# Kernel optimization log

Hardware: AMD Instinct MI355X
Metric: run time of the kernel (lower is better)

## Reference

```python
import jax, jax.numpy as jnp
import numpy as np

TOP_K = 3
EPS = 1e-12  # F.normalize eps


def _lstm(x, W_ih, W_hh, b_ih, b_hh):
    # x: [B, S, I]; PyTorch gate order i, f, g, o; returns h sequence [B, S, H]
    B = x.shape[0]
    H = W_hh.shape[1]
    xs = jnp.swapaxes(x, 0, 1)  # [S, B, I]
    x_proj = xs @ W_ih.T + b_ih + b_hh  # [S, B, 4H]

    def step(carry, xp):
        h, c = carry
        gates = xp + h @ W_hh.T
        i, f, g, o = jnp.split(gates, 4, axis=-1)
        i = jax.nn.sigmoid(i); f = jax.nn.sigmoid(f)
        g = jnp.tanh(g); o = jax.nn.sigmoid(o)
        c = f * c + i * g
        h = o * jnp.tanh(c)
        return (h, c), h

    init = (jnp.zeros((B, H), x.dtype), jnp.zeros((B, H), x.dtype))
    _, hs = jax.lax.scan(step, init, x_proj)
    return jnp.swapaxes(hs, 0, 1)  # [B, S, H]


def setup_inputs() -> dict:
    key = jax.random.key(0)
    ks = jax.random.split(key, 16)
    B, S, I, H, M, N, O = 4, 256, 512, 1024, 256, 65536, 512
    sc = 0.02
    return {
        "x": jax.random.normal(ks[0], (B, S, I), jnp.float32),
        "keys": jax.random.normal(ks[1], (N, M), jnp.float32),
        "values": jax.random.normal(ks[2], (N, M), jnp.float32),
        "importance": jnp.ones((N,), jnp.float32),
        "W_ih": jax.random.normal(ks[3], (4 * H, I), jnp.float32) * sc,
        "W_hh": jax.random.normal(ks[4], (4 * H, H), jnp.float32) * sc,
        "b_ih": jnp.zeros((4 * H,), jnp.float32),
        "b_hh": jnp.zeros((4 * H,), jnp.float32),
        "Wq": jax.random.normal(ks[5], (M, H), jnp.float32) * sc,
        "bq": jnp.zeros((M,), jnp.float32),
        "Wa": jax.random.normal(ks[6], (1, M), jnp.float32) * sc,
        "ba": jnp.zeros((1,), jnp.float32),
        "Wc": jax.random.normal(ks[7], (M, M), jnp.float32) * sc,
        "bc": jnp.zeros((M,), jnp.float32),
        "Wo": jax.random.normal(ks[8], (O, H + M), jnp.float32) * sc,
        "bo": jnp.zeros((O,), jnp.float32),
    }


def reference(x, keys, values, importance, W_ih, W_hh, b_ih, b_hh,
              Wq, bq, Wa, ba, Wc, bc, Wo, bo):
    # Controller LSTM over the whole sequence
    h = _lstm(x, W_ih, W_hh, b_ih, b_hh)  # [B, S, H]

    # Query projection and cosine similarity against the memory keys
    q = h @ Wq.T + bq  # [B, S, M]
    qn = q / jnp.maximum(jnp.linalg.norm(q, axis=-1, keepdims=True), EPS)
    kn = keys / jnp.maximum(jnp.linalg.norm(keys, axis=-1, keepdims=True), EPS)
    sim = jnp.einsum("bsm,nm->bsn", qn, kn) * importance  # [B, S, N]

    # Top-k retrieval and value gather
    _, top_idx = jax.lax.top_k(sim, TOP_K)  # [B, S, k]
    retrieved = values[top_idx]  # [B, S, k, M]

    # Learned attention over retrieved memories
    att_logits = (retrieved @ Wa.T + ba)[..., 0]  # [B, S, k]
    att = jax.nn.softmax(att_logits, axis=-1)
    mem = jnp.einsum("bsk,bskm->bsm", att, retrieved)
    mem = mem @ Wc.T + bc  # combine_layer

    out = jnp.concatenate([h, mem], axis=-1) @ Wo.T + bo  # [B, S, O]
    return out
```

## Files before the change

kernel.cpp:

```cpp
#include <hip/hip_runtime.h>
#include <hip/hip_bf16.h>
#include <cstdint>
#include <cstddef>

#define BB 4
#define SS 256
#define ID 512
#define HD 1024
#define MD 256
#define NKEY 65536
#define OD 512
#define ROWS 1024
#define NWG_LSTM 256
#define NTH_LSTM 256
#define KPB 2048
#define KSPLITS (NKEY / KPB)

typedef __attribute__((ext_vector_type(8))) short bf16x8;
typedef __attribute__((ext_vector_type(4))) float f32x4;
typedef __attribute__((ext_vector_type(8))) unsigned short u16x8;

__global__ __launch_bounds__(256) void sgemm_nt(
    const float* __restrict__ A, int lda,
    const float* __restrict__ Bm, int ldb,
    float* __restrict__ C, int ldc, int K,
    const float* __restrict__ bias, const float* __restrict__ bias2,
    int accum)
{
    __shared__ float As[64][17];
    __shared__ float Bs[64][17];
    const int t = threadIdx.x;
    const int tx = t & 15, ty = t >> 4;
    const int bm = blockIdx.y << 6, bn = blockIdx.x << 6;
    const int lrow = t >> 2, lk4 = (t & 3) << 2;
    float acc[4][4] = {};

    for (int kb = 0; kb < K; kb += 16) {
        const float4 av = *(const float4*)&A[(size_t)(bm + lrow) * lda + kb + lk4];
        const float4 bv = *(const float4*)&Bm[(size_t)(bn + lrow) * ldb + kb + lk4];
        __syncthreads();
        As[lrow][lk4 + 0] = av.x; As[lrow][lk4 + 1] = av.y;
        As[lrow][lk4 + 2] = av.z; As[lrow][lk4 + 3] = av.w;
        Bs[lrow][lk4 + 0] = bv.x; Bs[lrow][lk4 + 1] = bv.y;
        Bs[lrow][lk4 + 2] = bv.z; Bs[lrow][lk4 + 3] = bv.w;
        __syncthreads();
#pragma unroll
        for (int k = 0; k < 16; ++k) {
            const float a0 = As[4 * ty + 0][k], a1 = As[4 * ty + 1][k];
            const float a2 = As[4 * ty + 2][k], a3 = As[4 * ty + 3][k];
            const float b0 = Bs[4 * tx + 0][k], b1 = Bs[4 * tx + 1][k];
            const float b2 = Bs[4 * tx + 2][k], b3 = Bs[4 * tx + 3][k];
            acc[0][0] += a0 * b0; acc[0][1] += a0 * b1; acc[0][2] += a0 * b2; acc[0][3] += a0 * b3;
            acc[1][0] += a1 * b0; acc[1][1] += a1 * b1; acc[1][2] += a1 * b2; acc[1][3] += a1 * b3;
            acc[2][0] += a2 * b0; acc[2][1] += a2 * b1; acc[2][2] += a2 * b2; acc[2][3] += a2 * b3;
            acc[3][0] += a3 * b0; acc[3][1] += a3 * b1; acc[3][2] += a3 * b2; acc[3][3] += a3 * b3;
        }
    }

#pragma unroll
    for (int i = 0; i < 4; ++i) {
        const int row = bm + 4 * ty + i;
        const int col = bn + 4 * tx;
        float4* cp = (float4*)&C[(size_t)row * ldc + col];
        float4 r;
        if (accum) {
            const float4 old = *cp;
            r.x = old.x + acc[i][0]; r.y = old.y + acc[i][1];
            r.z = old.z + acc[i][2]; r.w = old.w + acc[i][3];
        } else {
            float bx = bias[col + 0], by = bias[col + 1], bz = bias[col + 2], bw = bias[col + 3];
            if (bias2) { bx += bias2[col + 0]; by += bias2[col + 1]; bz += bias2[col + 2]; bw += bias2[col + 3]; }
            r.x = acc[i][0] + bx; r.y = acc[i][1] + by;
            r.z = acc[i][2] + bz; r.w = acc[i][3] + bw;
        }
        *cp = r;
    }
}

__global__ __launch_bounds__(256) void sgemm_nt_w(
    const float* __restrict__ A, const float* __restrict__ Bm,
    float* __restrict__ C, const float* __restrict__ bias, const float* __restrict__ bias2)
{
    __shared__ float As[16][64];
    __shared__ float Bs[16][128];
    const int t = threadIdx.x;
    const int tx = t & 15, ty = t >> 4;
    const int bm = blockIdx.y << 6, bn = blockIdx.x << 7;
    const int arow = t & 63, akq = t >> 6;
    const int brow = t & 127, bkq = t >> 7;
    float acc[4][8] = {};

    for (int kb = 0; kb < 512; kb += 16) {
        const float4 av  = *(const float4*)&A[(size_t)(bm + arow) * 512 + kb + (akq << 2)];
        const float4 bv0 = *(const float4*)&Bm[(size_t)(bn + brow) * 512 + kb + (bkq << 3)];
        const float4 bv1 = *(const float4*)&Bm[(size_t)(bn + brow) * 512 + kb + (bkq << 3) + 4];
        __syncthreads();
        As[(akq << 2) + 0][arow] = av.x; As[(akq << 2) + 1][arow] = av.y;
        As[(akq << 2) + 2][arow] = av.z; As[(akq << 2) + 3][arow] = av.w;
        Bs[(bkq << 3) + 0][brow] = bv0.x; Bs[(bkq << 3) + 1][brow] = bv0.y;
        Bs[(bkq << 3) + 2][brow] = bv0.z; Bs[(bkq << 3) + 3][brow] = bv0.w;
        Bs[(bkq << 3) + 4][brow] = bv1.x; Bs[(bkq << 3) + 5][brow] = bv1.y;
        Bs[(bkq << 3) + 6][brow] = bv1.z; Bs[(bkq << 3) + 7][brow] = bv1.w;
        __syncthreads();
#pragma unroll
        for (int k = 0; k < 16; ++k) {
            const float4 a  = *(const float4*)&As[k][ty << 2];
            const float4 b0 = *(const float4*)&Bs[k][tx << 3];
            const float4 b1 = *(const float4*)&Bs[k][(tx << 3) + 4];
            acc[0][0] += a.x * b0.x; acc[0][1] += a.x * b0.y; acc[0][2] += a.x * b0.z; acc[0][3] += a.x * b0.w;
            acc[0][4] += a.x * b1.x; acc[0][5] += a.x * b1.y; acc[0][6] += a.x * b1.z; acc[0][7] += a.x * b1.w;
            acc[1][0] += a.y * b0.x; acc[1][1] += a.y * b0.y; acc[1][2] += a.y * b0.z; acc[1][3] += a.y * b0.w;
            acc[1][4] += a.y * b1.x; acc[1][5] += a.y * b1.y; acc[1][6] += a.y * b1.z; acc[1][7] += a.y * b1.w;
            acc[2][0] += a.z * b0.x; acc[2][1] += a.z * b0.y; acc[2][2] += a.z * b0.z; acc[2][3] += a.z * b0.w;
            acc[2][4] += a.z * b1.x; acc[2][5] += a.z * b1.y; acc[2][6] += a.z * b1.z; acc[2][7] += a.z * b1.w;
            acc[3][0] += a.w * b0.x; acc[3][1] += a.w * b0.y; acc[3][2] += a.w * b0.z; acc[3][3] += a.w * b0.w;
            acc[3][4] += a.w * b1.x; acc[3][5] += a.w * b1.y; acc[3][6] += a.w * b1.z; acc[3][7] += a.w * b1.w;
        }
    }

#pragma unroll
    for (int i = 0; i < 4; ++i) {
        const int row = bm + (ty << 2) + i;
        const int col = bn + (tx << 3);
        float4 r0, r1;
        r0.x = acc[i][0] + bias[col + 0] + bias2[col + 0];
        r0.y = acc[i][1] + bias[col + 1] + bias2[col + 1];
        r0.z = acc[i][2] + bias[col + 2] + bias2[col + 2];
        r0.w = acc[i][3] + bias[col + 3] + bias2[col + 3];
        r1.x = acc[i][4] + bias[col + 4] + bias2[col + 4];
        r1.y = acc[i][5] + bias[col + 5] + bias2[col + 5];
        r1.z = acc[i][6] + bias[col + 6] + bias2[col + 6];
        r1.w = acc[i][7] + bias[col + 7] + bias2[col + 7];
        *(float4*)&C[(size_t)row * 4096 + col] = r0;
        *(float4*)&C[(size_t)row * 4096 + col + 4] = r1;
    }
}

__device__ inline unsigned pack_bf16(float a, float b) {
    return (__float_as_uint(a) >> 16) | (__float_as_uint(b) & 0xFFFF0000u);
}

__global__ void rownorm(const float* __restrict__ X, float* __restrict__ Xn, int nrows)
{
    const int row = blockIdx.x * 4 + (threadIdx.x >> 6);
    const int lane = threadIdx.x & 63;
    if (row >= nrows) return;
    float4 v = *(const float4*)&X[(size_t)row * 256 + (lane << 2)];
    float ss = v.x * v.x + v.y * v.y + v.z * v.z + v.w * v.w;
#pragma unroll
    for (int o = 1; o < 64; o <<= 1) ss += __shfl_xor(ss, o);
    const float sc = 1.f / fmaxf(sqrtf(ss), 1e-12f);
    v.x *= sc; v.y *= sc; v.z *= sc; v.w *= sc;
    *(float4*)&Xn[(size_t)row * 256 + (lane << 2)] = v;
}

__device__ inline float sigm_f(float x) { return 1.f / (1.f + __expf(-x)); }
__device__ inline float tanh_f(float x) { return 1.f - 2.f / (__expf(2.f * x) + 1.f); }

#define SUBSTEP(B, U, UN, C4, XPC) do {                                           \
    asm volatile("s_waitcnt vmcnt(3)" ::: "memory");                              \
    __builtin_amdgcn_sched_barrier(0);                                            \
    const unsigned* pb_ = rec + (slot << 12) + (B << 10) + (t << 2);              \
    while ((((U.x ^ st) | (U.y ^ st) | (U.z ^ st) | (U.w ^ st)) & 0xFFu) != 0u) { \
        __builtin_amdgcn_s_sleep(1);                                              \
        asm volatile("global_load_dwordx4 %0, %1, off sc0 sc1\n\ts_waitcnt vmcnt(0)" \
                     : "=&v"(U) : "v"(pb_) : "memory");                           \
    }                                                                             \
    {                                                                             \
        float4 hw_;                                                               \
        hw_.x = __uint_as_float(U.x & 0xFFFFFF00u);                               \
        hw_.y = __uint_as_float(U.y & 0xFFFFFF00u);                               \
        hw_.z = __uint_as_float(U.z & 0xFFFFFF00u);                               \
        hw_.w = __uint_as_float(U.w & 0xFFFFFF00u);                               \
        *(float4*)&h_lds[B][t << 2] = hw_;                                        \
    }                                                                             \
    asm volatile("s_waitcnt lgkmcnt(0)" ::: "memory");                            \
    __builtin_amdgcn_sched_barrier(0);                                            \
    __builtin_amdgcn_s_barrier();                                                 \
    {                                                                             \
        const unsigned* pn_ = rec + (((B == 3) ? (slot ^ 1) : slot) << 12)        \
                              + (((B + 1) & 3) << 10) + (t << 2);                 \
        asm volatile("global_load_dwordx4 %0, %1, off sc0 sc1"                    \
                     : "=&v"(UN) : "v"(pn_) : "memory");                          \
    }                                                                             \
    const float* hb_ = &h_lds[B][0];                                              \
    float ax_ = 0.f, ay_ = 0.f, az_ = 0.f, aw_ = 0.f;                             \
    _Pragma("unroll")                                                             \
    for (int j = 0; j < 16; ++j) {                                                \
        const float4 hv_ = *(const float4*)&hb_[(ksub << 2) + (j << 6)];          \
        ax_ += w4[j].x * hv_.x; ay_ += w4[j].y * hv_.y;                           \
        az_ += w4[j].z * hv_.z; aw_ += w4[j].w * hv_.w;                           \
    }                                                                             \
    float sm_ = (ax_ + ay_) + (az_ + aw_);                                        \
    sm_ += __shfl_xor(sm_, 1); sm_ += __shfl_xor(sm_, 2);                         \
    sm_ += __shfl_xor(sm_, 4); sm_ += __shfl_xor(sm_, 8);                         \
    sm_ += XPC;                                                                   \
    const float vi_ = __shfl(sm_, ksub);                                          \
    const float vf_ = __shfl(sm_, ksub + 16);                                     \
    const float vg_ = __shfl(sm_, ksub + 32);                                     \
    const float vo_ = __shfl(sm_, ksub + 48);                                     \
    const float iv_ = sigm_f(vi_), fv_ = sigm_f(vf_);                             \
    const float gv_ = tanh_f(vg_), ov_ = sigm_f(vo_);                             \
    C4 = fv_ * C4 + iv_ * gv_;                                                    \
    const float hvv_ = ov_ * tanh_f(C4);                                          \
    if (lane == 0) {                                                              \
        unsigned* dst_ = rec + ((slot ^ 1) << 12) + (B << 10) + unit;             \
        const unsigned uv_ = (__float_as_uint(hvv_) & 0xFFFFFF00u) |              \
                             ((unsigned)(s + 1) & 0xFFu);                         \
        float* ha_ = &h_all[(size_t)((B << 8) + s) * 1024 + unit];                \
        asm volatile("global_store_dword %0, %1, off sc0 sc1"                     \
                     :: "v"(dst_), "v"(uv_) : "memory");                          \
        asm volatile("global_store_dword %0, %1, off"                             \
                     :: "v"(ha_), "v"(hvv_) : "memory");                          \
    }                                                                             \
    {                                                                             \
        const float* px_ = &xp[(size_t)((B << 8) + sn) * 4096 + wrow];            \
        asm volatile("global_load_dword %0, %1, off"                              \
                     : "=&v"(XPC) : "v"(px_) : "memory");                         \
    }                                                                             \
} while (0)

__global__ __launch_bounds__(256) void lstm_kernel(
    const float* __restrict__ xp, const float* __restrict__ W_hh,
    unsigned* __restrict__ rec, float* __restrict__ h_all,
    const float* __restrict__ keys, const float* __restrict__ imp,
    float* __restrict__ rnk, unsigned short* __restrict__ kb)
{
    __shared__ float h_lds[4][1024];
    const int t = threadIdx.x;

    if (blockIdx.x >= NWG_LSTM) {
        const int base_row = (blockIdx.x - NWG_LSTM) << 8;
        const int lane = t & 63;
        for (int it = 0; it < 64; ++it) {
            const int row = base_row + (it << 2) + (t >> 6);
            float4 v = *(const float4*)&keys[(size_t)row * 256 + (lane << 2)];
            float ss = v.x * v.x + v.y * v.y + v.z * v.z + v.w * v.w;
#pragma unroll
            for (int o = 1; o < 64; o <<= 1) ss += __shfl_xor(ss, o);
            const float sc = imp[row] / fmaxf(sqrtf(ss), 1e-12f);
            if (lane == 0) rnk[row] = sc;
            if (kb) {
                uint2 p;
                p.x = pack_bf16(v.x * sc, v.y * sc);
                p.y = pack_bf16(v.z * sc, v.w * sc);
                *(uint2*)&kb[(size_t)row * 256 + (lane << 2)] = p;
            }
        }
        return;
    }

    const int wave = t >> 6, lane = t & 63;
    const int gt = lane >> 4, ksub = lane & 15;
    const int unit = (blockIdx.x << 2) + wave;
    const int wrow = (gt << 10) + unit;

    float4 w4[16];
#pragma unroll
    for (int j = 0; j < 16; ++j)
        w4[j] = *(const float4*)&W_hh[(size_t)wrow * 1024 + (ksub << 2) + (j << 6)];

    float c40 = 0.f, c41 = 0.f, c42 = 0.f, c43 = 0.f;
    float xpc0 = xp[(size_t)(0 * 256 + 0) * 4096 + wrow];
    float xpc1 = xp[(size_t)(1 * 256 + 0) * 4096 + wrow];
    float xpc2 = xp[(size_t)(2 * 256 + 0) * 4096 + wrow];
    float xpc3 = xp[(size_t)(3 * 256 + 0) * 4096 + wrow];

    uint4 u0 = make_uint4(~0u, ~0u, ~0u, ~0u);
    uint4 u1 = u0, u2 = u0, u3 = u0;

    {
        const unsigned* p00 = rec + (t << 2);
        asm volatile("global_load_dwordx4 %0, %1, off sc0 sc1\n\ts_waitcnt vmcnt(0)"
                     : "=&v"(u0) : "v"(p00) : "memory");
        __builtin_amdgcn_sched_barrier(0);
    }

    for (int s = 0; s < 256; ++s) {
        const int slot = s & 1;
        const unsigned st = (unsigned)s & 0xFFu;
        const int sn = (s < 255) ? s + 1 : 255;
        SUBSTEP(0, u0, u1, c40, xpc0);
        SUBSTEP(1, u1, u2, c41, xpc1);
        SUBSTEP(2, u2, u3, c42, xpc2);
        SUBSTEP(3, u3, u0, c43, xpc3);
    }
}

#define SWAP1(A, B, IA, IB) { float _t = A; A = B; B = _t; int _u = IA; IA = IB; IB = _u; }
#define INS8G(P, V, ID) do {                                          \
    const float _v = (V); const int _id = (ID);                       \
    if (_v > P##v7) {                                                 \
        P##v7 = _v; P##i7 = _id;                                      \
        if (P##v7 > P##v6) SWAP1(P##v6, P##v7, P##i6, P##i7);         \
        if (P##v6 > P##v5) SWAP1(P##v5, P##v6, P##i5, P##i6);         \
        if (P##v5 > P##v4) SWAP1(P##v4, P##v5, P##i4, P##i5);         \
        if (P##v4 > P##v3) SWAP1(P##v3, P##v4, P##i3, P##i4);         \
        if (P##v3 > P##v2) SWAP1(P##v2, P##v3, P##i2, P##i3);         \
        if (P##v2 > P##v1) SWAP1(P##v1, P##v2, P##i1, P##i2);         \
        if (P##v1 > P##v0) SWAP1(P##v0, P##v1, P##i0, P##i1);         \
    }                                                                 \
} while (0)
#define DECL8(P) float P##v0=-3e38f,P##v1=-3e38f,P##v2=-3e38f,P##v3=-3e38f, \
                       P##v4=-3e38f,P##v5=-3e38f,P##v6=-3e38f,P##v7=-3e38f; \
                 int P##i0=0x7fffffff,P##i1=0x7fffffff,P##i2=0x7fffffff,P##i3=0x7fffffff, \
                     P##i4=0x7fffffff,P##i5=0x7fffffff,P##i6=0x7fffffff,P##i7=0x7fffffff;

__global__ __launch_bounds__(512) void sim_mfma_b8(
    const float* __restrict__ qn, const unsigned short* __restrict__ kb,
    float* __restrict__ part_v8, int* __restrict__ part_i8)
{
    __shared__ unsigned short k_lds[64 * 264];
    const int t = threadIdx.x;
    const int wave = t >> 6, lane = t & 63;
    const int ks = blockIdx.x, qs = blockIdx.y;
    const int key_base = ks * KPB;
    const int q0 = qs << 7;
    const int qrow = q0 + (wave << 4) + (lane & 15);
    const int kg = lane >> 4;

    bf16x8 bq[8];
#pragma unroll
    for (int kc = 0; kc < 8; ++kc) {
        const float* qp = &qn[(size_t)qrow * 256 + (kc << 5) + (kg << 3)];
        const float4 f0 = *(const float4*)qp;
        const float4 f1 = *(const float4*)(qp + 4);
        union { unsigned int u[4]; bf16x8 h; } cv;
        cv.u[0] = pack_bf16(f0.x, f0.y);
        cv.u[1] = pack_bf16(f0.z, f0.w);
        cv.u[2] = pack_bf16(f1.x, f1.y);
        cv.u[3] = pack_bf16(f1.z, f1.w);
        bq[kc] = cv.h;
    }

    DECL8(t)

    const int srow = t >> 3, scol0 = (t & 7) << 5;

    for (int stg = 0; stg < KPB / 64; ++stg) {
        __syncthreads();
        {
            const unsigned short* kp = &kb[(size_t)(key_base + (stg << 6) + srow) * 256 + scol0];
#pragma unroll
            for (int i = 0; i < 4; ++i)
                *(u16x8*)&k_lds[srow * 264 + scol0 + (i << 3)] = *(const u16x8*)(kp + (i << 3));
        }
        __syncthreads();

#pragma unroll
        for (int kt = 0; kt < 4; ++kt) {
            f32x4 a0 = {0.f, 0.f, 0.f, 0.f};
            f32x4 a1 = {0.f, 0.f, 0.f, 0.f};
#pragma unroll
            for (int kc = 0; kc < 4; ++kc) {
                const bf16x8 af = *(const bf16x8*)&k_lds[((kt << 4) + (lane & 15)) * 264 +
                                                         (kc << 5) + (kg << 3)];
                a0 = __builtin_amdgcn_mfma_f32_16x16x32_bf16(af, bq[kc], a0, 0, 0, 0);
            }
#pragma unroll
            for (int kc = 4; kc < 8; ++kc) {
                const bf16x8 af = *(const bf16x8*)&k_lds[((kt << 4) + (lane & 15)) * 264 +
                                                         (kc << 5) + (kg << 3)];
                a1 = __builtin_amdgcn_mfma_f32_16x16x32_bf16(af, bq[kc], a1, 0, 0, 0);
            }
            const int kidx = key_base + (stg << 6) + (kt << 4) + (kg << 2);
            INS8G(t, a0[0] + a1[0], kidx + 0);
            INS8G(t, a0[1] + a1[1], kidx + 1);
            INS8G(t, a0[2] + a1[2], kidx + 2);
            INS8G(t, a0[3] + a1[3], kidx + 3);
        }
    }

    float* cand_v = (float*)k_lds;
    int*   cand_i = (int*)(k_lds + 8192);
    __syncthreads();
    cand_v[t * 8 + 0] = tv0; cand_i[t * 8 + 0] = ti0;
    cand_v[t * 8 + 1] = tv1; cand_i[t * 8 + 1] = ti1;
    cand_v[t * 8 + 2] = tv2; cand_i[t * 8 + 2] = ti2;
    cand_v[t * 8 + 3] = tv3; cand_i[t * 8 + 3] = ti3;
    cand_v[t * 8 + 4] = tv4; cand_i[t * 8 + 4] = ti4;
    cand_v[t * 8 + 5] = tv5; cand_i[t * 8 + 5] = ti5;
    cand_v[t * 8 + 6] = tv6; cand_i[t * 8 + 6] = ti6;
    cand_v[t * 8 + 7] = tv7; cand_i[t * 8 + 7] = ti7;
    __syncthreads();
    if (t < 128) {
        DECL8(m)
        const int w = t >> 4, c = t & 15;
        for (int g = 0; g < 4; ++g) {
            const int src = ((w << 6) + (g << 4) + c) * 8;
            for (int r = 0; r < 8; ++r)
                INS8G(m, cand_v[src + r], cand_i[src + r]);
        }
        const size_t base = (size_t)(q0 + t) * (KSPLITS * 8) + ks * 8;
        part_v8[base + 0] = mv0; part_i8[base + 0] = mi0;
        part_v8[base + 1] = mv1; part_i8[base + 1] = mi1;
        part_v8[base + 2] = mv2; part_i8[base + 2] = mi2;
        part_v8[base + 3] = mv3; part_i8[base + 3] = mi3;
        part_v8[base + 4] = mv4; part_i8[base + 4] = mi4;
        part_v8[base + 5] = mv5; part_i8[base + 5] = mi5;
        part_v8[base + 6] = mv6; part_i8[base + 6] = mi6;
        part_v8[base + 7] = mv7; part_i8[base + 7] = mi7;
    }
}

__global__ __launch_bounds__(256) void sim_mfma_f(
    const float* __restrict__ qn, const float* __restrict__ keys,
    const float* __restrict__ rnk, float* __restrict__ part_v8, int* __restrict__ part_i8)
{
    __shared__ unsigned short k_lds[64 * 264];
    __shared__ float cand_v[256 * 8];
    __shared__ int   cand_i[256 * 8];
    const int t = threadIdx.x;
    const int wave = t >> 6, lane = t & 63;
    const int ks = blockIdx.x, qs = blockIdx.y;
    const int key_base = ks * KPB;
    const int q0 = qs << 6;
    const int qrow = q0 + (wave << 4) + (lane & 15);
    const int kg = lane >> 4;

    bf16x8 bq[8];
#pragma unroll
    for (int kc = 0; kc < 8; ++kc) {
        const float* qp = &qn[(size_t)qrow * 256 + (kc << 5) + (kg << 3)];
        const float4 f0 = *(const float4*)qp;
        const float4 f1 = *(const float4*)(qp + 4);
        union { unsigned int u[4]; bf16x8 h; } cv;
        cv.u[0] = pack_bf16(f0.x, f0.y);
        cv.u[1] = pack_bf16(f0.z, f0.w);
        cv.u[2] = pack_bf16(f1.x, f1.y);
        cv.u[3] = pack_bf16(f1.z, f1.w);
        bq[kc] = cv.h;
    }

    DECL8(t)

    for (int stg = 0; stg < KPB / 64; ++stg) {
        __syncthreads();
#pragma unroll
        for (int i = 0; i < 8; ++i) {
            const int g = (i << 11) + (t << 3);
            const int row = g >> 8, col = g & 255;
            const int krow = key_base + (stg << 6) + row;
            const float sc = rnk[krow];
            const float* kp = &keys[(size_t)krow * 256 + col];
            float4 f0 = *(const float4*)kp;
            float4 f1 = *(const float4*)(kp + 4);
            f0.x *= sc; f0.y *= sc; f0.z *= sc; f0.w *= sc;
            f1.x *= sc; f1.y *= sc; f1.z *= sc; f1.w *= sc;
            union { unsigned int u[4]; u16x8 h; } cv;
            cv.u[0] = pack_bf16(f0.x, f0.y);
            cv.u[1] = pack_bf16(f0.z, f0.w);
            cv.u[2] = pack_bf16(f1.x, f1.y);
            cv.u[3] = pack_bf16(f1.z, f1.w);
            *(u16x8*)&k_lds[row * 264 + col] = cv.h;
        }
        __syncthreads();

#pragma unroll
        for (int kt = 0; kt < 4; ++kt) {
            f32x4 a0 = {0.f, 0.f, 0.f, 0.f};
            f32x4 a1 = {0.f, 0.f, 0.f, 0.f};
#pragma unroll
            for (int kc = 0; kc < 4; ++kc) {
                const bf16x8 af = *(const bf16x8*)&k_lds[((kt << 4) + (lane & 15)) * 264 +
                                                         (kc << 5) + (kg << 3)];
                a0 = __builtin_amdgcn_mfma_f32_16x16x32_bf16(af, bq[kc], a0, 0, 0, 0);
            }
#pragma unroll
            for (int kc = 4; kc < 8; ++kc) {
                const bf16x8 af = *(const bf16x8*)&k_lds[((kt << 4) + (lane & 15)) * 264 +
                                                         (kc << 5) + (kg << 3)];
                a1 = __builtin_amdgcn_mfma_f32_16x16x32_bf16(af, bq[kc], a1, 0, 0, 0);
            }
            const int kidx = key_base + (stg << 6) + (kt << 4) + (kg << 2);
            INS8G(t, a0[0] + a1[0], kidx + 0);
            INS8G(t, a0[1] + a1[1], kidx + 1);
            INS8G(t, a0[2] + a1[2], kidx + 2);
            INS8G(t, a0[3] + a1[3], kidx + 3);
        }
    }

    __syncthreads();
    cand_v[t * 8 + 0] = tv0; cand_i[t * 8 + 0] = ti0;
    cand_v[t * 8 + 1] = tv1; cand_i[t * 8 + 1] = ti1;
    cand_v[t * 8 + 2] = tv2; cand_i[t * 8 + 2] = ti2;
    cand_v[t * 8 + 3] = tv3; cand_i[t * 8 + 3] = ti3;
    cand_v[t * 8 + 4] = tv4; cand_i[t * 8 + 4] = ti4;
    cand_v[t * 8 + 5] = tv5; cand_i[t * 8 + 5] = ti5;
    cand_v[t * 8 + 6] = tv6; cand_i[t * 8 + 6] = ti6;
    cand_v[t * 8 + 7] = tv7; cand_i[t * 8 + 7] = ti7;
    __syncthreads();
    if (t < 64) {
        DECL8(m)
        const int w = t >> 4, c = t & 15;
        for (int g = 0; g < 4; ++g) {
            const int src = ((w << 6) + c + (g << 4)) * 8;
            for (int r = 0; r < 8; ++r)
                INS8G(m, cand_v[src + r], cand_i[src + r]);
        }
        const size_t base = (size_t)(q0 + t) * (KSPLITS * 8) + ks * 8;
        part_v8[base + 0] = mv0; part_i8[base + 0] = mi0;
        part_v8[base + 1] = mv1; part_i8[base + 1] = mi1;
        part_v8[base + 2] = mv2; part_i8[base + 2] = mi2;
        part_v8[base + 3] = mv3; part_i8[base + 3] = mi3;
        part_v8[base + 4] = mv4; part_i8[base + 4] = mi4;
        part_v8[base + 5] = mv5; part_i8[base + 5] = mi5;
        part_v8[base + 6] = mv6; part_i8[base + 6] = mi6;
        part_v8[base + 7] = mv7; part_i8[base + 7] = mi7;
    }
}

__global__ __launch_bounds__(256) void cand_merge(
    const float* __restrict__ part_v8, const int* __restrict__ part_i8,
    int* __restrict__ cand8_i)
{
    __shared__ float pv[256 * 8];
    __shared__ int   pi[256 * 8];
    const int t = threadIdx.x;
    const int qq = t >> 3, sl = t & 7;
    const int q = (blockIdx.x << 5) + qq;
    {
        DECL8(p)
        const size_t base = (size_t)q * (KSPLITS * 8) + sl * 32;
        for (int j = 0; j < 32; ++j)
            INS8G(p, part_v8[base + j], part_i8[base + j]);
        pv[t * 8 + 0] = pv0; pi[t * 8 + 0] = pi0;
        pv[t * 8 + 1] = pv1; pi[t * 8 + 1] = pi1;
        pv[t * 8 + 2] = pv2; pi[t * 8 + 2] = pi2;
        pv[t * 8 + 3] = pv3; pi[t * 8 + 3] = pi3;
        pv[t * 8 + 4] = pv4; pi[t * 8 + 4] = pi4;
        pv[t * 8 + 5] = pv5; pi[t * 8 + 5] = pi5;
        pv[t * 8 + 6] = pv6; pi[t * 8 + 6] = pi6;
        pv[t * 8 + 7] = pv7; pi[t * 8 + 7] = pi7;
    }
    __syncthreads();
    if (sl == 0) {
        DECL8(c)
        const int b0 = (qq << 3) * 8;
        for (int j = 0; j < 64; ++j)
            INS8G(c, pv[b0 + j], pi[b0 + j]);
        cand8_i[q * 8 + 0] = ci0; cand8_i[q * 8 + 1] = ci1;
        cand8_i[q * 8 + 2] = ci2; cand8_i[q * 8 + 3] = ci3;
        cand8_i[q * 8 + 4] = ci4; cand8_i[q * 8 + 5] = ci5;
        cand8_i[q * 8 + 6] = ci6; cand8_i[q * 8 + 7] = ci7;
    }
}

__global__ void rescore_gather(const float* __restrict__ qn, const float* __restrict__ keys,
                               const float* __restrict__ rnk, const int* __restrict__ cand8_i,
                               const float* __restrict__ values, const float* __restrict__ Wa,
                               const float* __restrict__ ba, float* __restrict__ mem_raw)
{
    const int q = blockIdx.x;
    const int lane = threadIdx.x;
    const float4 qv = *(const float4*)&qn[(size_t)q * 256 + (lane << 2)];
    float s0, s1, s2, s3, s4, s5, s6, s7;
    int j0, j1, j2, j3, j4, j5, j6, j7;
#define RES(R, S, J) { J = cand8_i[q * 8 + R]; \
    const float4 kv = *(const float4*)&keys[(size_t)J * 256 + (lane << 2)]; \
    float d = qv.x * kv.x + qv.y * kv.y + qv.z * kv.z + qv.w * kv.w; \
    d += __shfl_xor(d, 1); d += __shfl_xor(d, 2); d += __shfl_xor(d, 4); \
    d += __shfl_xor(d, 8); d += __shfl_xor(d, 16); d += __shfl_xor(d, 32); \
    S = d * rnk[J]; }
    RES(0, s0, j0) RES(1, s1, j1) RES(2, s2, j2) RES(3, s3, j3)
    RES(4, s4, j4) RES(5, s5, j5) RES(6, s6, j6) RES(7, s7, j7)
#undef RES
    int top[3];
#define BET(SV, JV) if (SV > bv || (SV == bv && JV < bi)) { bv = SV; bi = JV; }
#pragma unroll
    for (int k = 0; k < 3; ++k) {
        float bv = s0; int bi = j0;
        BET(s1, j1) BET(s2, j2) BET(s3, j3) BET(s4, j4)
        BET(s5, j5) BET(s6, j6) BET(s7, j7)
        top[k] = bi;
        if (j0 == bi) s0 = -3e38f;
        if (j1 == bi) s1 = -3e38f;
        if (j2 == bi) s2 = -3e38f;
        if (j3 == bi) s3 = -3e38f;
        if (j4 == bi) s4 = -3e38f;
        if (j5 == bi) s5 = -3e38f;
        if (j6 == bi) s6 = -3e38f;
        if (j7 == bi) s7 = -3e38f;
    }
#undef BET
    const float4 wa = *(const float4*)&Wa[lane << 2];
    float4 vr[3];
    float lg[3];
#pragma unroll
    for (int r = 0; r < 3; ++r) {
        const float4 v = *(const float4*)&values[(size_t)top[r] * 256 + (lane << 2)];
        vr[r] = v;
        float d = v.x * wa.x + v.y * wa.y + v.z * wa.z + v.w * wa.w;
#pragma unroll
        for (int o = 1; o < 64; o <<= 1) d += __shfl_xor(d, o);
        lg[r] = d + ba[0];
    }
    const float mx = fmaxf(lg[0], fmaxf(lg[1], lg[2]));
    float e0 = __expf(lg[0] - mx), e1 = __expf(lg[1] - mx), e2 = __expf(lg[2] - mx);
    const float inv = 1.f / (e0 + e1 + e2);
    e0 *= inv; e1 *= inv; e2 *= inv;
    float4 m;
    m.x = e0 * vr[0].x + e1 * vr[1].x + e2 * vr[2].x;
    m.y = e0 * vr[0].y + e1 * vr[1].y + e2 * vr[2].y;
    m.z = e0 * vr[0].z + e1 * vr[1].z + e2 * vr[2].z;
    m.w = e0 * vr[0].w + e1 * vr[1].w + e2 * vr[2].w;
    *(float4*)&mem_raw[(size_t)q * 256 + (lane << 2)] = m;
}

__global__ __launch_bounds__(256) void gemm_bf16_nt(
    const float* __restrict__ in1, int K1,
    const float* __restrict__ in2, int K2,
    const float* __restrict__ Wm,
    float* __restrict__ C, int N,
    const float* __restrict__ bias)
{
    __shared__ unsigned short a_lds[64 * 72];
    __shared__ unsigned short w_lds[64 * 72];
    const int t = threadIdx.x;
    const int wave = t >> 6, lane = t & 63;
    const int bn = blockIdx.x << 6, bm = blockIdx.y << 6;
    const int kg = lane >> 4;
    const int K = K1 + K2;

    f32x4 acc0 = {0.f, 0.f, 0.f, 0.f};
    f32x4 acc1 = {0.f, 0.f, 0.f, 0.f};
    f32x4 acc2 = {0.f, 0.f, 0.f, 0.f};
    f32x4 acc3 = {0.f, 0.f, 0.f, 0.f};

    const int srow = t >> 2, sc0 = (t & 3) << 4;

    for (int kb = 0; kb < K; kb += 64) {
        __syncthreads();
        {
            const float* src; int ld; int col = kb + sc0;
            if (col < K1) { src = in1; ld = K1; } else { src = in2; ld = K2; col -= K1; }
            const float* p = &src[(size_t)(bm + srow) * ld + col];
#pragma unroll
            for (int i = 0; i < 4; ++i) {
                const float4 f = *(const float4*)(p + (i << 2));
                uint2 pk;
                pk.x = pack_bf16(f.x, f.y);
                pk.y = pack_bf16(f.z, f.w);
                *(uint2*)&a_lds[srow * 72 + sc0 + (i << 2)] = pk;
            }
            const float* pw = &Wm[(size_t)(bn + srow) * K + kb + sc0];
#pragma unroll
            for (int i = 0; i < 4; ++i) {
                const float4 f = *(const float4*)(pw + (i << 2));
                uint2 pk;
                pk.x = pack_bf16(f.x, f.y);
                pk.y = pack_bf16(f.z, f.w);
                *(uint2*)&w_lds[srow * 72 + sc0 + (i << 2)] = pk;
            }
        }
        __syncthreads();

#pragma unroll
        for (int ks = 0; ks < 2; ++ks) {
            const int koff = (ks << 5) + (kg << 3);
            const bf16x8 af = *(const bf16x8*)&w_lds[((wave << 4) + (lane & 15)) * 72 + koff];
            const bf16x8 b0 = *(const bf16x8*)&a_lds[((0 << 4) + (lane & 15)) * 72 + koff];
            const bf16x8 b1 = *(const bf16x8*)&a_lds[((1 << 4) + (lane & 15)) * 72 + koff];
            const bf16x8 b2 = *(const bf16x8*)&a_lds[((2 << 4) + (lane & 15)) * 72 + koff];
            const bf16x8 b3 = *(const bf16x8*)&a_lds[((3 << 4) + (lane & 15)) * 72 + koff];
            acc0 = __builtin_amdgcn_mfma_f32_16x16x32_bf16(af, b0, acc0, 0, 0, 0);
            acc1 = __builtin_amdgcn_mfma_f32_16x16x32_bf16(af, b1, acc1, 0, 0, 0);
            acc2 = __builtin_amdgcn_mfma_f32_16x16x32_bf16(af, b2, acc2, 0, 0, 0);
            acc3 = __builtin_amdgcn_mfma_f32_16x16x32_bf16(af, b3, acc3, 0, 0, 0);
        }
    }

    const int ncol = bn + (wave << 4) + (kg << 2);
    const float4 bv = *(const float4*)&bias[ncol];
#define EPI(MQ, ACC) do {                                              \
        const int m_ = bm + (MQ << 4) + (lane & 15);                   \
        float4 r_;                                                     \
        r_.x = ACC[0] + bv.x; r_.y = ACC[1] + bv.y;                    \
        r_.z = ACC[2] + bv.z; r_.w = ACC[3] + bv.w;                    \
        *(float4*)&C[(size_t)m_ * N + ncol] = r_;                      \
    } while (0)
    EPI(0, acc0);
    EPI(1, acc1);
    EPI(2, acc2);
    EPI(3, acc3);
#undef EPI
}

extern "C" void kernel_launch(void* const* d_in, const int* in_sizes, int n_in,
                              void* d_out, int out_size, void* d_ws, size_t ws_size,
                              hipStream_t stream)
{
    (void)in_sizes; (void)n_in; (void)out_size;
    const float* x     = (const float*)d_in[0];
    const float* keys  = (const float*)d_in[1];
    const float* values= (const float*)d_in[2];
    const float* imp   = (const float*)d_in[3];
    const float* W_ih  = (const float*)d_in[4];
    const float* W_hh  = (const float*)d_in[5];
    const float* b_ih  = (const float*)d_in[6];
    const float* b_hh  = (const float*)d_in[7];
    const float* Wq    = (const float*)d_in[8];
    const float* bq    = (const float*)d_in[9];
    const float* Wa    = (const float*)d_in[10];
    const float* ba    = (const float*)d_in[11];
    const float* Wc    = (const float*)d_in[12];
    const float* bc    = (const float*)d_in[13];
    const float* Wo    = (const float*)d_in[14];
    const float* bo    = (const float*)d_in[15];
    float* out = (float*)d_out;

    float* ws = (float*)d_ws;
    size_t o = 0;
    float* xp      = ws + o; o += (size_t)1024 * 4096;
    float* h_all   = ws + o; o += (size_t)1024 * 1024;
    unsigned* rec  = (unsigned*)(ws + o); o += 2 * 4096;
    float* rnk     = ws + o; o += NKEY;
    float* qbuf    = ws + o; o += (size_t)ROWS * 256;
    float* qn      = ws + o; o += (size_t)ROWS * 256;
    float* part_v8 = ws + o; o += (size_t)ROWS * KSPLITS * 8;
    int*   part_i8 = (int*)(ws + o); o += (size_t)ROWS * KSPLITS * 8;
    int*   cand8_i = (int*)(ws + o); o += ROWS * 8;
    float* mem_raw = ws + o; o += (size_t)ROWS * 256;
    float* memb    = ws + o; o += (size_t)ROWS * 256;
    unsigned short* kb = (unsigned short*)(ws + o);
    const size_t need_bf16 = (o + (size_t)NKEY * 256 / 2) * sizeof(float);
    const bool use_bf16 = ws_size >= need_bf16;

    hipMemsetAsync(rec, 0, 2 * 4096 * 4, stream);

    sgemm_nt_w<<<dim3(32, 16), 256, 0, stream>>>(x, W_ih, xp, b_ih, b_hh);

    lstm_kernel<<<2 * NWG_LSTM, NTH_LSTM, 0, stream>>>(
        xp, W_hh, rec, h_all, keys, imp, rnk, use_bf16 ? kb : nullptr);

    sgemm_nt<<<dim3(4, 16), 256, 0, stream>>>(h_all, HD, Wq, HD, qbuf, MD, HD, bq, nullptr, 0);

    rownorm<<<ROWS / 4, 256, 0, stream>>>(qbuf, qn, ROWS);

    if (use_bf16)
        sim_mfma_b8<<<dim3(KSPLITS, 8), 512, 0, stream>>>(qn, kb, part_v8, part_i8);
    else
        sim_mfma_f<<<dim3(KSPLITS, 16), 256, 0, stream>>>(qn, keys, rnk, part_v8, part_i8);
    cand_merge<<<32, 256, 0, stream>>>(part_v8, part_i8, cand8_i);
    rescore_gather<<<ROWS, 64, 0, stream>>>(qn, keys, rnk, cand8_i, values, Wa, ba, mem_raw);

    gemm_bf16_nt<<<dim3(4, 16), 256, 0, stream>>>(mem_raw, MD, nullptr, 0, Wc, memb, MD, bc);

    gemm_bf16_nt<<<dim3(8, 16), 256, 0, stream>>>(h_all, HD, memb, MD, Wo, out, OD, bo);
}
```

Before: 1.188 ms.

## Switch similarity kernel to 32x32x16 MFMA with 256-thread blocks and smaller key splits

Rewrites the bf16 similarity top-k kernel to use 32x32x16 MFMA instructions, with each wave covering 32 queries against 64 keys per stage, instead of 16x16x32 tiles. Blocks shrink to 256 threads with two blocks per CU, and the key chunk per block halves so the grid doubles. cand_merge is adjusted to merge twice as many partial candidates per query. The aim is fewer LDS reads per MFMA and better occupancy, at the cost of more registers per thread (16 query fragments, two 16-wide accumulators) and more merge work.

```diff
diff --git a/kernel.cpp b/kernel.cpp
--- a/kernel.cpp
+++ b/kernel.cpp
@@ -13,11 +13,12 @@
 #define ROWS 1024
 #define NWG_LSTM 256
 #define NTH_LSTM 256
-#define KPB 2048
+#define KPB 1024
 #define KSPLITS (NKEY / KPB)
 
 typedef __attribute__((ext_vector_type(8))) short bf16x8;
 typedef __attribute__((ext_vector_type(4))) float f32x4;
+typedef __attribute__((ext_vector_type(16))) float f32x16;
 typedef __attribute__((ext_vector_type(8))) unsigned short u16x8;
 
 __global__ __launch_bounds__(256) void sgemm_nt(
@@ -306,7 +307,7 @@
                  int P##i0=0x7fffffff,P##i1=0x7fffffff,P##i2=0x7fffffff,P##i3=0x7fffffff, \
                      P##i4=0x7fffffff,P##i5=0x7fffffff,P##i6=0x7fffffff,P##i7=0x7fffffff;
 
-__global__ __launch_bounds__(512) void sim_mfma_b8(
+__global__ __launch_bounds__(256, 2) void sim_mfma_b32(
     const float* __restrict__ qn, const unsigned short* __restrict__ kb,
     float* __restrict__ part_v8, int* __restrict__ part_i8)
 {
@@ -316,13 +317,13 @@
     const int ks = blockIdx.x, qs = blockIdx.y;
     const int key_base = ks * KPB;
     const int q0 = qs << 7;
-    const int qrow = q0 + (wave << 4) + (lane & 15);
-    const int kg = lane >> 4;
-
-    bf16x8 bq[8];
-#pragma unroll
-    for (int kc = 0; kc < 8; ++kc) {
-        const float* qp = &qn[(size_t)qrow * 256 + (kc << 5) + (kg << 3)];
+    const int qrow = q0 + (wave << 5) + (lane & 31);
+    const int kh = lane >> 5;
+
+    bf16x8 bq[16];
+#pragma unroll
+    for (int kc = 0; kc < 16; ++kc) {
+        const float* qp = &qn[(size_t)qrow * 256 + (kc << 4) + (kh << 3)];
         const float4 f0 = *(const float4*)qp;
         const float4 f1 = *(const float4*)(qp + 4);
         union { unsigned int u[4]; bf16x8 h; } cv;
@@ -335,44 +336,40 @@
 
     DECL8(t)
 
-    const int srow = t >> 3, scol0 = (t & 7) << 5;
+    const int srow = t >> 2, sc0 = (t & 3) << 6;
 
     for (int stg = 0; stg < KPB / 64; ++stg) {
         __syncthreads();
         {
-            const unsigned short* kp = &kb[(size_t)(key_base + (stg << 6) + srow) * 256 + scol0];
-#pragma unroll
-            for (int i = 0; i < 4; ++i)
-                *(u16x8*)&k_lds[srow * 264 + scol0 + (i << 3)] = *(const u16x8*)(kp + (i << 3));
-        }
-        __syncthreads();
-
-#pragma unroll
-        for (int kt = 0; kt < 4; ++kt) {
-            f32x4 a0 = {0.f, 0.f, 0.f, 0.f};
-            f32x4 a1 = {0.f, 0.f, 0.f, 0.f};
-#pragma unroll
-            for (int kc = 0; kc < 4; ++kc) {
-                const bf16x8 af = *(const bf16x8*)&k_lds[((kt << 4) + (lane & 15)) * 264 +
-                                                         (kc << 5) + (kg << 3)];
-                a0 = __builtin_amdgcn_mfma_f32_16x16x32_bf16(af, bq[kc], a0, 0, 0, 0);
-            }
-#pragma unroll
-            for (int kc = 4; kc < 8; ++kc) {
-                const bf16x8 af = *(const bf16x8*)&k_lds[((kt << 4) + (lane & 15)) * 264 +
-                                                         (kc << 5) + (kg << 3)];
-                a1 = __builtin_amdgcn_mfma_f32_16x16x32_bf16(af, bq[kc], a1, 0, 0, 0);
-            }
-            const int kidx = key_base + (stg << 6) + (kt << 4) + (kg << 2);
-            INS8G(t, a0[0] + a1[0], kidx + 0);
-            INS8G(t, a0[1] + a1[1], kidx + 1);
-            INS8G(t, a0[2] + a1[2], kidx + 2);
-            INS8G(t, a0[3] + a1[3], kidx + 3);
-        }
+            const unsigned short* kp = &kb[(size_t)(key_base + (stg << 6) + srow) * 256 + sc0];
+#pragma unroll
+            for (int i = 0; i < 8; ++i)
+                *(u16x8*)&k_lds[srow * 264 + sc0 + (i << 3)] = *(const u16x8*)(kp + (i << 3));
+        }
+        __syncthreads();
+
+        f32x16 a0 = {0.f};
+        f32x16 a1 = {0.f};
+#pragma unroll
+        for (int kc = 0; kc < 16; ++kc) {
+            const int col = (kc << 4) + (kh << 3);
+            const bf16x8 k0 = *(const bf16x8*)&k_lds[((lane & 31)) * 264 + col];
+            const bf16x8 k1 = *(const bf16x8*)&k_lds[(32 + (lane & 31)) * 264 + col];
+            a0 = __builtin_amdgcn_mfma_f32_32x32x16_bf16(k0, bq[kc], a0, 0, 0, 0);
+            a1 = __builtin_amdgcn_mfma_f32_32x32x16_bf16(k1, bq[kc], a1, 0, 0, 0);
+        }
+
+        const int kb0 = key_base + (stg << 6) + (kh << 2);
+#define INSROW(ACC, BASE, R) INS8G(t, ACC[R], (BASE) + ((R) & 3) + (((R) >> 2) << 3))
+#pragma unroll
+        for (int r = 0; r < 16; ++r) INSROW(a0, kb0, r);
+#pragma unroll
+        for (int r = 0; r < 16; ++r) INSROW(a1, kb0 + 32, r);
+#undef INSROW
     }
 
     float* cand_v = (float*)k_lds;
-    int*   cand_i = (int*)(k_lds + 8192);
+    int*   cand_i = (int*)(k_lds + 4096);
     __syncthreads();
     cand_v[t * 8 + 0] = tv0; cand_i[t * 8 + 0] = ti0;
     cand_v[t * 8 + 1] = tv1; cand_i[t * 8 + 1] = ti1;
@@ -385,12 +382,11 @@
     __syncthreads();
     if (t < 128) {
         DECL8(m)
-        const int w = t >> 4, c = t & 15;
-        for (int g = 0; g < 4; ++g) {
-            const int src = ((w << 6) + (g << 4) + c) * 8;
-            for (int r = 0; r < 8; ++r)
-                INS8G(m, cand_v[src + r], cand_i[src + r]);
-        }
+        const int w = t >> 5, c = t & 31;
+        const int s0 = ((w << 6) + c) * 8;
+        const int s1 = ((w << 6) + 32 + c) * 8;
+        for (int r = 0; r < 8; ++r) INS8G(m, cand_v[s0 + r], cand_i[s0 + r]);
+        for (int r = 0; r < 8; ++r) INS8G(m, cand_v[s1 + r], cand_i[s1 + r]);
         const size_t base = (size_t)(q0 + t) * (KSPLITS * 8) + ks * 8;
         part_v8[base + 0] = mv0; part_i8[base + 0] = mi0;
         part_v8[base + 1] = mv1; part_i8[base + 1] = mi1;
@@ -521,8 +517,8 @@
     const int q = (blockIdx.x << 5) + qq;
     {
         DECL8(p)
-        const size_t base = (size_t)q * (KSPLITS * 8) + sl * 32;
-        for (int j = 0; j < 32; ++j)
+        const size_t base = (size_t)q * (KSPLITS * 8) + sl * 64;
+        for (int j = 0; j < 64; ++j)
             INS8G(p, part_v8[base + j], part_i8[base + j]);
         pv[t * 8 + 0] = pv0; pi[t * 8 + 0] = pi0;
         pv[t * 8 + 1] = pv1; pi[t * 8 + 1] = pi1;
@@ -738,7 +734,7 @@
     rownorm<<<ROWS / 4, 256, 0, stream>>>(qbuf, qn, ROWS);
 
     if (use_bf16)
-        sim_mfma_b8<<<dim3(KSPLITS, 8), 512, 0, stream>>>(qn, kb, part_v8, part_i8);
+        sim_mfma_b32<<<dim3(KSPLITS, 8), 256, 0, stream>>>(qn, kb, part_v8, part_i8);
     else
         sim_mfma_f<<<dim3(KSPLITS, 16), 256, 0, stream>>>(qn, keys, rnk, part_v8, part_i8);
     cand_merge<<<32, 256, 0, stream>>>(part_v8, part_i8, cand8_i);
```

New measurement: 1.183 ms. Within noise of the previous version (-0.4%).
